# Kernel tuning notes

Measured on AMD Instinct MI355X. Metric: run time of the kernel, lower is better.

## Reference

```python
import jax, jax.numpy as jnp
import numpy as np

ALPHA = 0.2
NEG_INF = -9e15


def setup_inputs() -> dict:
    key = jax.random.key(0)
    k1, k2, k3, k4 = jax.random.split(key, 4)
    N, F_IN, F_OUT, H = 4096, 1, 64, 12
    x = jax.random.normal(k1, (N, F_IN), dtype=jnp.float32)
    adj = jax.random.randint(k2, (N, N), 0, 2).astype(jnp.int32)
    # per-head params stacked: W [H, F_IN, F_OUT], a [H, 2*F_OUT, 1]
    W = jax.random.normal(k3, (H, F_IN, F_OUT), dtype=jnp.float32) * 0.1
    a = jax.random.normal(k4, (H, 2 * F_OUT, 1), dtype=jnp.float32) * 0.1
    return {"x": x, "adj": adj, "W": W, "a": a}


def reference(x, adj, W, a):
    # h per head: [H, N, F_OUT]
    h = jnp.einsum('nf,hfo->hno', x, W)
    F_out = h.shape[-1]
    # a_input[i,j] = concat(h_i, h_j), so a_input @ a = h_i.a_src + h_j.a_dst
    a_src = a[:, :F_out, 0]   # [H, F_OUT]
    a_dst = a[:, F_out:, 0]   # [H, F_OUT]
    e_src = jnp.einsum('hnf,hf->hn', h, a_src)  # [H, N]
    e_dst = jnp.einsum('hnf,hf->hn', h, a_dst)  # [H, N]
    e = jax.nn.leaky_relu(e_src[:, :, None] + e_dst[:, None, :], ALPHA)  # [H,N,N]
    e = jnp.where(adj[None] > 0, e, NEG_INF)
    attn = jax.nn.softmax(e, axis=-1)           # softmax over neighbors j
    h_prime = jnp.einsum('hij,hjf->hif', attn, h)  # [H, N, F_OUT]
    # concat heads along feature dim -> [N, H*F_OUT]
    N = h_prime.shape[1]
    return jnp.transpose(h_prime, (1, 0, 2)).reshape(N, -1)
```

## Files before the change

### kernel.cpp

```cpp
#include <hip/hip_runtime.h>

#define GAT_H 12
#define GAT_N 4096
#define GAT_F 64
#define LOG2E 1.4426950408889634f


__device__ float g_tab2[GAT_H * GAT_N];
__device__ float g_sd[2 * GAT_H + 1];

__global__ __launch_bounds__(256) void gat_prep(const float* __restrict__ W,
                                                const float* __restrict__ a,
                                                const float* __restrict__ x) {
    const int b    = blockIdx.x;
    const int tid  = threadIdx.x;
    const int lane = tid & 63;
    const int wave = tid >> 6;

    if (b < GAT_H) {
        if (wave == 0) {
            const float wf = W[b * GAT_F + lane];
            float ps = wf * a[b * 2 * GAT_F + lane];
            float pd = wf * a[b * 2 * GAT_F + GAT_F + lane];
            #pragma unroll
            for (int off = 32; off > 0; off >>= 1) {
                ps += __shfl_xor(ps, off, 64);
                pd += __shfl_xor(pd, off, 64);
            }
            if (lane == 0) { g_sd[b] = ps; g_sd[GAT_H + b] = pd; }
        }
        return;
    }
    if (b == GAT_H) {
        if (wave == 0) {
            float s = 0.0f;
            #pragma unroll
            for (int j = 0; j < GAT_N / 64; ++j) s += x[j * 64 + lane];
            #pragma unroll
            for (int off = 32; off > 0; off >>= 1) s += __shfl_xor(s, off, 64);
            if (lane == 0) g_sd[2 * GAT_H] = s * (1.0f / GAT_N);
        }
        return;
    }

    const int bt    = b - (GAT_H + 1);
    const int h     = bt >> 2;
    const int chunk = bt & 3;
    const float wf  = W[h * GAT_F + lane];
    float pd = wf * a[h * 2 * GAT_F + GAT_F + lane];
    #pragma unroll
    for (int off = 32; off > 0; off >>= 1) pd += __shfl_xor(pd, off, 64);
    const float dl5 = 0.2f * pd * LOG2E;
    #pragma unroll
    for (int k = 0; k < 4; ++k) {
        const int j = chunk * 1024 + k * 256 + tid;
        g_tab2[h * GAT_N + j] = __builtin_amdgcn_exp2f(dl5 * x[j]);
    }
}

__global__ __launch_bounds__(512) void gat_main(const float* __restrict__ x,
                                                const int* __restrict__ adj,
                                                const float* __restrict__ W,
                                                float* __restrict__ out) {
    __shared__ float xs[GAT_N];
    __shared__ float rho_s[4][16];
    __shared__ float part[2][2][4][6][2];
    __shared__ float cbuf[4][GAT_H];

    const int tid  = threadIdx.x;
    const int row0 = blockIdx.x * 4;

    #pragma unroll
    for (int it = 0; it < GAT_N / (512 * 4); ++it)
        ((float4*)xs)[it * 512 + tid] = ((const float4*)x)[it * 512 + tid];
    if (tid < 64) {
        const int r = tid >> 4, hh = tid & 15;
        if (hh < GAT_H)
            rho_s[r][hh] =
                __builtin_amdgcn_exp2f(-0.8f * LOG2E * x[row0 + r] * g_sd[hh]);
    }
    __syncthreads();

    const int lane  = tid & 63;
    const int wave  = tid >> 6;
    const int rp    = wave >> 2;
    const int hg    = (wave >> 1) & 1;
    const int jh    = wave & 1;
    const int hbase = hg * 6;

    float rho[2][6];
    #pragma unroll
    for (int r = 0; r < 2; ++r)
        #pragma unroll
        for (int hh = 0; hh < 6; ++hh)
            rho[r][hh] = __uint_as_float(__builtin_amdgcn_readfirstlane(
                __float_as_uint(rho_s[rp * 2 + r][hbase + hh])));

    float den[2][6], num[2][6];
    #pragma unroll
    for (int r = 0; r < 2; ++r)
        #pragma unroll
        for (int hh = 0; hh < 6; ++hh) { den[r][hh] = 0.0f; num[r][hh] = 0.0f; }

    const int4*   __restrict__ a4p =
        (const int4*)(adj + (size_t)(row0 + rp * 2) * GAT_N + jh * 2048);
    const float4* __restrict__ t4 =
        (const float4*)(g_tab2 + hbase * GAT_N + jh * 2048);
    const float4* __restrict__ x4 = (const float4*)(xs + jh * 2048);

    #pragma unroll 1
    for (int it = 0; it < 8; ++it) {
        const int idx = it * 64 + lane;
        const int4   a0 = a4p[idx];
        const int4   a1 = a4p[(GAT_N / 4) + idx];
        const float4 xv = x4[idx];

        const int*   ai0 = (const int*)&a0;
        const int*   ai1 = (const int*)&a1;
        const float* xp  = (const float*)&xv;
        float am[2][4], axj[2][4];
        #pragma unroll
        for (int e = 0; e < 4; ++e) {
            am[0][e]  = (float)ai0[e];
            am[1][e]  = (float)ai1[e];
            axj[0][e] = am[0][e] * xp[e];
            axj[1][e] = am[1][e] * xp[e];
        }

        #pragma unroll
        for (int hh = 0; hh < 6; ++hh) {
            const float4 e2v = t4[hh * (GAT_N / 4) + idx];
            const float* e2  = (const float*)&e2v;
            #pragma unroll
            for (int e = 0; e < 4; ++e) {
                const float w  = e2[e] * e2[e];
                const float w4 = w * w;
                #pragma unroll
                for (int r = 0; r < 2; ++r) {
                    const float p = fmaxf(w4, rho[r][hh]) * e2[e];
                    den[r][hh] = fmaf(p, am[r][e],  den[r][hh]);
                    num[r][hh] = fmaf(p, axj[r][e], num[r][hh]);
                }
            }
        }
    }

    #pragma unroll
    for (int r = 0; r < 2; ++r) {
        #pragma unroll
        for (int hh = 0; hh < 6; ++hh) {
            float d = den[r][hh], n = num[r][hh];
            #pragma unroll
            for (int off = 32; off > 0; off >>= 1) {
                d += __shfl_xor(d, off, 64);
                n += __shfl_xor(n, off, 64);
            }
            if (lane == 0) {
                part[jh][hg][rp * 2 + r][hh][0] = d;
                part[jh][hg][rp * 2 + r][hh][1] = n;
            }
        }
    }
    __syncthreads();

    if (tid < 64) {
        const int r = tid >> 4, h = tid & 15;
        if (h < GAT_H) {
            const int g  = (h >= 6) ? 1 : 0;
            const int hh = h - 6 * g;
            const float dsum = part[0][g][r][hh][0] + part[1][g][r][hh][0];
            const float nsum = part[0][g][r][hh][1] + part[1][g][r][hh][1];
            cbuf[r][h] = dsum > 0.0f ? nsum / dsum : g_sd[2 * GAT_H];
        }
    }
    __syncthreads();

    #pragma unroll
    for (int r = 0; r < 4; ++r) {
        const size_t base = (size_t)(row0 + r) * (GAT_H * GAT_F);
        #pragma unroll
        for (int k = 0; k < 2; ++k) {
            const int pos = k * 512 + tid;
            if (pos < GAT_H * GAT_F)
                out[base + pos] = cbuf[r][pos >> 6] * W[pos];
        }
    }
}

extern "C" void kernel_launch(void* const* d_in, const int* in_sizes, int n_in,
                              void* d_out, int out_size, void* d_ws, size_t ws_size,
                              hipStream_t stream) {
    const float* x   = (const float*)d_in[0];
    const int*   adj = (const int*)d_in[1];
    const float* W   = (const float*)d_in[2];
    const float* a   = (const float*)d_in[3];
    float* out = (float*)d_out;
    (void)d_ws; (void)ws_size;

    gat_prep<<<GAT_H + 1 + 48, 256, 0, stream>>>(W, a, x);
    gat_main<<<GAT_N / 4, 512, 0, stream>>>(x, adj, W, out);
}
```

Before: 143.2 us.

## Stage exp table through double-buffered LDS and prefetch adjacency per row

Restructures the main kernel so each wave handles one row and six heads over the full neighbor range. The exp table chunk for all twelve heads is staged cooperatively into double-buffered shared memory, and the next adjacency and x chunk is prefetched while the current one is processed. The cross-wave partial reduction through shared memory goes away. The cost is a block-wide barrier every iteration and each thread doing only a single row's work per table load, which lowers register reuse of the table values compared with handling two rows per load.

```diff
diff --git a/kernel.cpp b/kernel.cpp
--- a/kernel.cpp
+++ b/kernel.cpp
@@ -62,127 +62,115 @@
                                                 const int* __restrict__ adj,
                                                 const float* __restrict__ W,
                                                 float* __restrict__ out) {
-    __shared__ float xs[GAT_N];
-    __shared__ float rho_s[4][16];
-    __shared__ float part[2][2][4][6][2];
+    __shared__ float tab_lds[2][GAT_H][256];
     __shared__ float cbuf[4][GAT_H];
 
-    const int tid  = threadIdx.x;
-    const int row0 = blockIdx.x * 4;
+    const int tid   = threadIdx.x;
+    const int row0  = blockIdx.x * 4;
+    const int lane  = tid & 63;
+    const int wave  = tid >> 6;
+    const int r     = wave >> 1;
+    const int hg    = wave & 1;
+    const int hbase = hg * 6;
+    const int row   = row0 + r;
+
+    const float xrow = x[row];
+    float rho[6];
+    #pragma unroll
+    for (int hh = 0; hh < 6; ++hh)
+        rho[hh] = __uint_as_float(__builtin_amdgcn_readfirstlane(__float_as_uint(
+            __builtin_amdgcn_exp2f(-0.8f * LOG2E * xrow * g_sd[hbase + hh]))));
+
+    float den[6], num[6];
+    #pragma unroll
+    for (int hh = 0; hh < 6; ++hh) { den[hh] = 0.0f; num[hh] = 0.0f; }
+
+    const float2* __restrict__ tg = (const float2*)g_tab2;
+    int sh[3], sj[3];
+    #pragma unroll
+    for (int k = 0; k < 3; ++k) {
+        const int p = k * 512 + tid;
+        sh[k] = p >> 7;
+        sj[k] = p & 127;
+    }
+    float2* __restrict__ lds2 = (float2*)tab_lds;
 
     #pragma unroll
-    for (int it = 0; it < GAT_N / (512 * 4); ++it)
-        ((float4*)xs)[it * 512 + tid] = ((const float4*)x)[it * 512 + tid];
-    if (tid < 64) {
-        const int r = tid >> 4, hh = tid & 15;
-        if (hh < GAT_H)
-            rho_s[r][hh] =
-                __builtin_amdgcn_exp2f(-0.8f * LOG2E * x[row0 + r] * g_sd[hh]);
-    }
+    for (int k = 0; k < 3; ++k)
+        lds2[sh[k] * 128 + sj[k]] = tg[sh[k] * (GAT_N / 2) + sj[k]];
+    const int4*   __restrict__ a4p = (const int4*)(adj + (size_t)row * GAT_N);
+    const float4* __restrict__ x4  = (const float4*)x;
+    int4   a_c = a4p[lane];
+    float4 x_c = x4[lane];
     __syncthreads();
 
-    const int lane  = tid & 63;
-    const int wave  = tid >> 6;
-    const int rp    = wave >> 2;
-    const int hg    = (wave >> 1) & 1;
-    const int jh    = wave & 1;
-    const int hbase = hg * 6;
+    #pragma unroll 2
+    for (int it = 0; it < 16; ++it) {
+        const int buf = it & 1;
+        const int nit = (it < 15) ? it + 1 : 15;
 
-    float rho[2][6];
-    #pragma unroll
-    for (int r = 0; r < 2; ++r)
+        float2 st[3];
         #pragma unroll
-        for (int hh = 0; hh < 6; ++hh)
-            rho[r][hh] = __uint_as_float(__builtin_amdgcn_readfirstlane(
-                __float_as_uint(rho_s[rp * 2 + r][hbase + hh])));
+        for (int k = 0; k < 3; ++k)
+            st[k] = tg[sh[k] * (GAT_N / 2) + nit * 128 + sj[k]];
+        const int ni = nit * 64 + lane;
+        const int4   a_n = a4p[ni];
+        const float4 x_n = x4[ni];
 
-    float den[2][6], num[2][6];
-    #pragma unroll
-    for (int r = 0; r < 2; ++r)
-        #pragma unroll
-        for (int hh = 0; hh < 6; ++hh) { den[r][hh] = 0.0f; num[r][hh] = 0.0f; }
-
-    const int4*   __restrict__ a4p =
-        (const int4*)(adj + (size_t)(row0 + rp * 2) * GAT_N + jh * 2048);
-    const float4* __restrict__ t4 =
-        (const float4*)(g_tab2 + hbase * GAT_N + jh * 2048);
-    const float4* __restrict__ x4 = (const float4*)(xs + jh * 2048);
-
-    #pragma unroll 1
-    for (int it = 0; it < 8; ++it) {
-        const int idx = it * 64 + lane;
-        const int4   a0 = a4p[idx];
-        const int4   a1 = a4p[(GAT_N / 4) + idx];
-        const float4 xv = x4[idx];
-
-        const int*   ai0 = (const int*)&a0;
-        const int*   ai1 = (const int*)&a1;
-        const float* xp  = (const float*)&xv;
-        float am[2][4], axj[2][4];
+        const int*   ai = (const int*)&a_c;
+        const float* xp = (const float*)&x_c;
+        float am[4], axj[4];
         #pragma unroll
         for (int e = 0; e < 4; ++e) {
-            am[0][e]  = (float)ai0[e];
-            am[1][e]  = (float)ai1[e];
-            axj[0][e] = am[0][e] * xp[e];
-            axj[1][e] = am[1][e] * xp[e];
+            am[e]  = (float)ai[e];
+            axj[e] = am[e] * xp[e];
         }
 
         #pragma unroll
         for (int hh = 0; hh < 6; ++hh) {
-            const float4 e2v = t4[hh * (GAT_N / 4) + idx];
+            const float4 e2v = *(const float4*)&tab_lds[buf][hbase + hh][4 * lane];
             const float* e2  = (const float*)&e2v;
             #pragma unroll
             for (int e = 0; e < 4; ++e) {
                 const float w  = e2[e] * e2[e];
                 const float w4 = w * w;
-                #pragma unroll
-                for (int r = 0; r < 2; ++r) {
-                    const float p = fmaxf(w4, rho[r][hh]) * e2[e];
-                    den[r][hh] = fmaf(p, am[r][e],  den[r][hh]);
-                    num[r][hh] = fmaf(p, axj[r][e], num[r][hh]);
-                }
+                const float p  = fmaxf(w4, rho[hh]) * e2[e];
+                den[hh] = fmaf(p, am[e],  den[hh]);
+                num[hh] = fmaf(p, axj[e], num[hh]);
             }
         }
+
+        #pragma unroll
+        for (int k = 0; k < 3; ++k)
+            lds2[(buf ^ 1) * (GAT_H * 128) + sh[k] * 128 + sj[k]] = st[k];
+        a_c = a_n; x_c = x_n;
+        __syncthreads();
     }
 
     #pragma unroll
-    for (int r = 0; r < 2; ++r) {
+    for (int hh = 0; hh < 6; ++hh) {
         #pragma unroll
-        for (int hh = 0; hh < 6; ++hh) {
-            float d = den[r][hh], n = num[r][hh];
-            #pragma unroll
-            for (int off = 32; off > 0; off >>= 1) {
-                d += __shfl_xor(d, off, 64);
-                n += __shfl_xor(n, off, 64);
-            }
-            if (lane == 0) {
-                part[jh][hg][rp * 2 + r][hh][0] = d;
-                part[jh][hg][rp * 2 + r][hh][1] = n;
-            }
+        for (int off = 32; off > 0; off >>= 1) {
+            den[hh] += __shfl_xor(den[hh], off, 64);
+            num[hh] += __shfl_xor(num[hh], off, 64);
         }
     }
-    __syncthreads();
-
-    if (tid < 64) {
-        const int r = tid >> 4, h = tid & 15;
-        if (h < GAT_H) {
-            const int g  = (h >= 6) ? 1 : 0;
-            const int hh = h - 6 * g;
-            const float dsum = part[0][g][r][hh][0] + part[1][g][r][hh][0];
-            const float nsum = part[0][g][r][hh][1] + part[1][g][r][hh][1];
-            cbuf[r][h] = dsum > 0.0f ? nsum / dsum : g_sd[2 * GAT_H];
-        }
+    if (lane == 0) {
+        const float fb = g_sd[2 * GAT_H];
+        #pragma unroll
+        for (int hh = 0; hh < 6; ++hh)
+            cbuf[r][hbase + hh] = den[hh] > 0.0f ? num[hh] / den[hh] : fb;
     }
     __syncthreads();
 
     #pragma unroll
-    for (int r = 0; r < 4; ++r) {
-        const size_t base = (size_t)(row0 + r) * (GAT_H * GAT_F);
+    for (int rr = 0; rr < 4; ++rr) {
+        const size_t base = (size_t)(row0 + rr) * (GAT_H * GAT_F);
         #pragma unroll
         for (int k = 0; k < 2; ++k) {
             const int pos = k * 512 + tid;
             if (pos < GAT_H * GAT_F)
-                out[base + pos] = cbuf[r][pos >> 6] * W[pos];
+                out[base + pos] = cbuf[rr][pos >> 6] * W[pos];
         }
     }
 }
```

Measured after the change: 135.4 us. 5.5% less time.

## Software-pipeline adjacency and table loads in registers; drop LDS staging of x

Applied to the files above, without the earlier changes.

The main loop now uses register double-buffering. Adjacency rows are prefetched two iterations ahead, and the exp table and x values one iteration ahead, so global loads overlap with the arithmetic. The shared-memory copy of x and the rho staging plus the barrier are removed; x is read straight from global memory and rho is computed per wave. This raises register pressure, which may reduce occupancy, and the tail iterations issue redundant loads.

```diff
diff --git a/kernel.cpp b/kernel.cpp
--- a/kernel.cpp
+++ b/kernel.cpp
@@ -58,29 +58,55 @@
     }
 }
 
+#define GAT_ITER(B, IT)                                                        \
+    do {                                                                       \
+        float am[2][4], axj[2][4];                                             \
+        {                                                                      \
+            const int*   ai0 = (const int*)&aBuf[B][0];                        \
+            const int*   ai1 = (const int*)&aBuf[B][1];                        \
+            const float* xp  = (const float*)&xBuf[B];                         \
+            _Pragma("unroll")                                                  \
+            for (int e = 0; e < 4; ++e) {                                      \
+                am[0][e]  = (float)ai0[e];                                     \
+                am[1][e]  = (float)ai1[e];                                     \
+                axj[0][e] = am[0][e] * xp[e];                                  \
+                axj[1][e] = am[1][e] * xp[e];                                  \
+            }                                                                  \
+        }                                                                      \
+        const int i2_ = (((IT) < 6) ? (IT) + 2 : 7) * 64 + lane;               \
+        aBuf[B][0] = a4p0[i2_];                                                \
+        aBuf[B][1] = a4p1[i2_];                                                \
+        const int i1_ = (((IT) < 7) ? (IT) + 1 : 7) * 64 + lane;               \
+        _Pragma("unroll")                                                      \
+        for (int hh = 0; hh < 6; ++hh)                                         \
+            tBuf[(B) ^ 1][hh] = t4[hh * (GAT_N / 4) + i1_];                    \
+        xBuf[(B) ^ 1] = x4[i1_];                                               \
+        _Pragma("unroll")                                                      \
+        for (int hh = 0; hh < 6; ++hh) {                                       \
+            const float* e2 = (const float*)&tBuf[B][hh];                      \
+            _Pragma("unroll")                                                  \
+            for (int e = 0; e < 4; ++e) {                                      \
+                const float w  = e2[e] * e2[e];                                \
+                const float w4 = w * w;                              \
+                const float p0 = fmaxf(w4, rho[0][hh]) * e2[e];                \
+                const float p1 = fmaxf(w4, rho[1][hh]) * e2[e];                \
+                den[0][hh] = fmaf(p0, am[0][e],  den[0][hh]);                  \
+                num[0][hh] = fmaf(p0, axj[0][e], num[0][hh]);                  \
+                den[1][hh] = fmaf(p1, am[1][e],  den[1][hh]);                  \
+                num[1][hh] = fmaf(p1, axj[1][e], num[1][hh]);                  \
+            }                                                                  \
+        }                                                                      \
+    } while (0)
+
 __global__ __launch_bounds__(512) void gat_main(const float* __restrict__ x,
                                                 const int* __restrict__ adj,
                                                 const float* __restrict__ W,
                                                 float* __restrict__ out) {
-    __shared__ float xs[GAT_N];
-    __shared__ float rho_s[4][16];
     __shared__ float part[2][2][4][6][2];
     __shared__ float cbuf[4][GAT_H];
 
-    const int tid  = threadIdx.x;
-    const int row0 = blockIdx.x * 4;
-
-    #pragma unroll
-    for (int it = 0; it < GAT_N / (512 * 4); ++it)
-        ((float4*)xs)[it * 512 + tid] = ((const float4*)x)[it * 512 + tid];
-    if (tid < 64) {
-        const int r = tid >> 4, hh = tid & 15;
-        if (hh < GAT_H)
-            rho_s[r][hh] =
-                __builtin_amdgcn_exp2f(-0.8f * LOG2E * x[row0 + r] * g_sd[hh]);
-    }
-    __syncthreads();
-
+    const int tid   = threadIdx.x;
+    const int row0  = blockIdx.x * 4;
     const int lane  = tid & 63;
     const int wave  = tid >> 6;
     const int rp    = wave >> 2;
@@ -90,11 +116,14 @@
 
     float rho[2][6];
     #pragma unroll
-    for (int r = 0; r < 2; ++r)
+    for (int r = 0; r < 2; ++r) {
+        const float xr = x[row0 + rp * 2 + r];
         #pragma unroll
         for (int hh = 0; hh < 6; ++hh)
             rho[r][hh] = __uint_as_float(__builtin_amdgcn_readfirstlane(
-                __float_as_uint(rho_s[rp * 2 + r][hbase + hh])));
+                __float_as_uint(__builtin_amdgcn_exp2f(
+                    -0.8f * LOG2E * xr * g_sd[hbase + hh]))));
+    }
 
     float den[2][6], num[2][6];
     #pragma unroll
@@ -102,47 +131,26 @@
         #pragma unroll
         for (int hh = 0; hh < 6; ++hh) { den[r][hh] = 0.0f; num[r][hh] = 0.0f; }
 
-    const int4*   __restrict__ a4p =
+    const int4* __restrict__ a4p0 =
         (const int4*)(adj + (size_t)(row0 + rp * 2) * GAT_N + jh * 2048);
+    const int4* __restrict__ a4p1 = a4p0 + (GAT_N / 4);
     const float4* __restrict__ t4 =
         (const float4*)(g_tab2 + hbase * GAT_N + jh * 2048);
-    const float4* __restrict__ x4 = (const float4*)(xs + jh * 2048);
-
-    #pragma unroll 1
-    for (int it = 0; it < 8; ++it) {
-        const int idx = it * 64 + lane;
-        const int4   a0 = a4p[idx];
-        const int4   a1 = a4p[(GAT_N / 4) + idx];
-        const float4 xv = x4[idx];
-
-        const int*   ai0 = (const int*)&a0;
-        const int*   ai1 = (const int*)&a1;
-        const float* xp  = (const float*)&xv;
-        float am[2][4], axj[2][4];
-        #pragma unroll
-        for (int e = 0; e < 4; ++e) {
-            am[0][e]  = (float)ai0[e];
-            am[1][e]  = (float)ai1[e];
-            axj[0][e] = am[0][e] * xp[e];
-            axj[1][e] = am[1][e] * xp[e];
-        }
-
-        #pragma unroll
-        for (int hh = 0; hh < 6; ++hh) {
-            const float4 e2v = t4[hh * (GAT_N / 4) + idx];
-            const float* e2  = (const float*)&e2v;
-            #pragma unroll
-            for (int e = 0; e < 4; ++e) {
-                const float w  = e2[e] * e2[e];
-                const float w4 = w * w;
-                #pragma unroll
-                for (int r = 0; r < 2; ++r) {
-                    const float p = fmaxf(w4, rho[r][hh]) * e2[e];
-                    den[r][hh] = fmaf(p, am[r][e],  den[r][hh]);
-                    num[r][hh] = fmaf(p, axj[r][e], num[r][hh]);
-                }
-            }
-        }
+    const float4* __restrict__ x4 = (const float4*)(x + jh * 2048);
+
+    int4   aBuf[2][2];
+    float4 tBuf[2][6];
+    float4 xBuf[2];
+
+    aBuf[0][0] = a4p0[lane];      aBuf[0][1] = a4p1[lane];
+    aBuf[1][0] = a4p0[64 + lane]; aBuf[1][1] = a4p1[64 + lane];
+    #pragma unroll
+    for (int hh = 0; hh < 6; ++hh) tBuf[0][hh] = t4[hh * (GAT_N / 4) + lane];
+    xBuf[0] = x4[lane];
+
+    for (int k = 0; k < 4; ++k) {
+        GAT_ITER(0, 2 * k);
+        GAT_ITER(1, 2 * k + 1);
     }
 
     #pragma unroll
@@ -176,13 +184,13 @@
     __syncthreads();
 
     #pragma unroll
-    for (int r = 0; r < 4; ++r) {
-        const size_t base = (size_t)(row0 + r) * (GAT_H * GAT_F);
+    for (int rr = 0; rr < 4; ++rr) {
+        const size_t base = (size_t)(row0 + rr) * (GAT_H * GAT_F);
         #pragma unroll
         for (int k = 0; k < 2; ++k) {
             const int pos = k * 512 + tid;
             if (pos < GAT_H * GAT_F)
-                out[base + pos] = cbuf[r][pos >> 6] * W[pos];
+                out[base + pos] = cbuf[rr][pos >> 6] * W[pos];
         }
     }
 }
```

New measurement: 142.8 us. No clear change (-0.3%).
